# Kernel optimization log

Hardware: AMD Instinct MI355X
Metric: run time of the kernel (lower is better)

The kernel has to match this reference:

```python
import jax, jax.numpy as jnp
import numpy as np

D = 256; NH = 8; NL = 4; NP = 4; DFF = 1024
SHAPES = [(100, 100), (50, 50), (25, 25), (13, 13)]
B = 4


def layer_norm(x, g, b, eps=1e-5):
    m = x.mean(-1, keepdims=True)
    v = ((x - m) ** 2).mean(-1, keepdims=True)
    return (x - m) * jax.lax.rsqrt(v + eps) * g + b


def setup_inputs() -> dict:
    key = jax.random.key(0)
    ks = jax.random.split(key, 12)
    Lin = sum(h * w for h, w in SHAPES)  # 13294
    w = lambda k, s: jax.random.normal(k, s, jnp.float32) * 0.02
    return dict(
        src=jax.random.normal(ks[0], (B, Lin, D), jnp.float32),
        pos=0.1 * jax.random.normal(ks[1], (B, Lin, D), jnp.float32),
        reference_points=jax.random.uniform(ks[2], (B, Lin, NL, 2), dtype=jnp.float32),
        spatial_shapes=jnp.array(SHAPES, jnp.int32),
        level_start_index=jnp.array(np.cumsum([0] + [h * w for h, w in SHAPES])[:-1], jnp.int32),
        value_w=w(ks[3], (D, D)), value_b=jnp.zeros((D,), jnp.float32),
        offs_w=w(ks[4], (D, NH * NL * NP * 2)),
        offs_b=0.5 * jax.random.normal(ks[5], (NH * NL * NP * 2,), jnp.float32),
        attn_w=w(ks[6], (D, NH * NL * NP)), attn_b=jnp.zeros((NH * NL * NP,), jnp.float32),
        out_w=w(ks[7], (D, D)), out_b=jnp.zeros((D,), jnp.float32),
        ln1_g=jnp.ones((D,), jnp.float32), ln1_b=jnp.zeros((D,), jnp.float32),
        ff1_w=w(ks[8], (D, DFF)), ff1_b=jnp.zeros((DFF,), jnp.float32),
        ff2_w=w(ks[9], (DFF, D)), ff2_b=jnp.zeros((D,), jnp.float32),
        ln2_g=jnp.ones((D,), jnp.float32), ln2_b=jnp.zeros((D,), jnp.float32),
    )


def msda(query, value_in, ref, shapes, starts, value_w, value_b, offs_w, offs_b,
         attn_w, attn_b, out_w, out_b):
    Bq, Lq, Dm = query.shape
    dh = Dm // NH
    shapes_np = np.asarray(shapes); starts_np = np.asarray(starts)
    value = (value_in @ value_w + value_b).reshape(Bq, -1, NH, dh)
    offs = (query @ offs_w + offs_b).reshape(Bq, Lq, NH, NL, NP, 2)
    aw = jax.nn.softmax((query @ attn_w + attn_b).reshape(Bq, Lq, NH, NL * NP), axis=-1)
    aw = aw.reshape(Bq, Lq, NH, NL, NP)
    # offset normalizer is (W, H) per level
    normalizer = jnp.stack([shapes[:, 1], shapes[:, 0]], -1).astype(jnp.float32)
    loc = ref[:, :, None, :, None, :] + offs / normalizer[None, None, None, :, None, :]
    out = jnp.zeros((Bq, NH, Lq, dh), jnp.float32)
    for l in range(NL):
        Hl, Wl = int(shapes_np[l, 0]), int(shapes_np[l, 1])
        s = int(starts_np[l])
        v = value[:, s:s + Hl * Wl].transpose(0, 2, 1, 3)  # [B,h,HW,dh]
        x = loc[:, :, :, l, :, 0] * Wl - 0.5  # [B,Lq,h,P], align_corners=False
        y = loc[:, :, :, l, :, 1] * Hl - 0.5
        x0 = jnp.floor(x); y0 = jnp.floor(y)
        dx = x - x0; dy = y - y0
        x0i = x0.astype(jnp.int32); y0i = y0.astype(jnp.int32)
        def gather(ix, iy):
            valid = (ix >= 0) & (ix < Wl) & (iy >= 0) & (iy < Hl)  # zero padding
            idx = jnp.clip(iy, 0, Hl - 1) * Wl + jnp.clip(ix, 0, Wl - 1)
            idx = idx.transpose(0, 2, 1, 3).reshape(Bq, NH, Lq * NP)
            g = jnp.take_along_axis(v, idx[..., None], axis=2).reshape(Bq, NH, Lq, NP, dh)
            return g * valid.transpose(0, 2, 1, 3)[..., None]
        dxh = dx.transpose(0, 2, 1, 3)[..., None]
        dyh = dy.transpose(0, 2, 1, 3)[..., None]
        sampled = (gather(x0i, y0i) * (1 - dxh) * (1 - dyh)
                   + gather(x0i + 1, y0i) * dxh * (1 - dyh)
                   + gather(x0i, y0i + 1) * (1 - dxh) * dyh
                   + gather(x0i + 1, y0i + 1) * dxh * dyh)  # [B,h,Lq,P,dh]
        awl = aw[:, :, :, l].transpose(0, 2, 1, 3)[..., None]  # [B,h,Lq,P,1]
        out = out + (sampled * awl).sum(3)
    out = out.transpose(0, 2, 1, 3).reshape(Bq, Lq, Dm)
    return out @ out_w + out_b


def reference(src, pos, reference_points, spatial_shapes, level_start_index,
              value_w, value_b, offs_w, offs_b, attn_w, attn_b, out_w, out_b,
              ln1_g, ln1_b, ff1_w, ff1_b, ff2_w, ff2_b, ln2_g, ln2_b):
    # src = with_pos_embed(src, pos): NOTE this module uses (src + pos) as BOTH query and value
    q = src + pos
    src2 = msda(q, q, reference_points, spatial_shapes, level_start_index,
                value_w, value_b, offs_w, offs_b, attn_w, attn_b, out_w, out_b)
    x = layer_norm(q + src2, ln1_g, ln1_b)  # dropout is identity at eval
    ff = jnp.maximum(x @ ff1_w + ff1_b, 0.0) @ ff2_w + ff2_b
    return layer_norm(x + ff, ln2_g, ln2_b)
```

## Files before the change

kernel.cpp:

```cpp
#include <hip/hip_runtime.h>
#include <hip/hip_bf16.h>

#define B_    4
#define LIN   13294
#define M_    (B_*LIN)
#define D_    256
#define NH_   8
#define NL_   4
#define NP_   4
#define DFF_  1024

typedef __bf16 bf16;
typedef unsigned int uint;
typedef __attribute__((ext_vector_type(8))) __bf16 bfrag8;
typedef __attribute__((ext_vector_type(4))) __bf16 bf16x4;
typedef __attribute__((ext_vector_type(4))) float facc4;
typedef __attribute__((ext_vector_type(2))) float f32x2;

__global__ __launch_bounds__(256) void make_q(const float* __restrict__ src,
                                              const float* __restrict__ pos,
                                              float* __restrict__ q,
                                              bf16* __restrict__ qb, int n4) {
  int i = blockIdx.x * 256 + threadIdx.x;
  if (i >= n4) return;
  float4 s = ((const float4*)src)[i];
  float4 p = ((const float4*)pos)[i];
  float4 v = {s.x + p.x, s.y + p.y, s.z + p.z, s.w + p.w};
  ((float4*)q)[i] = v;
  bf16 t4[4] = {(bf16)v.x, (bf16)v.y, (bf16)v.z, (bf16)v.w};
  ((uint2*)qb)[i] = *(uint2*)t4;
}

__global__ __launch_bounds__(256) void prep_weights(
    const float* __restrict__ vw, const float* __restrict__ ow,
    const float* __restrict__ aw, const float* __restrict__ outw,
    const float* __restrict__ f1w, const float* __restrict__ f2w,
    const float* __restrict__ ob, const float* __restrict__ ab,
    bf16* __restrict__ vwt, bf16* __restrict__ oawt, bf16* __restrict__ outwt,
    bf16* __restrict__ f1wt, bf16* __restrict__ f2wt, float* __restrict__ oabias) {
  int seg = blockIdx.y;
  int idx = blockIdx.x * 256 + threadIdx.x;
  if (seg == 6) {
    if (idx < 256) oabias[idx] = ob[idx];
    else if (idx < 384) oabias[idx] = ab[idx - 256];
    return;
  }
  const float* W; bf16* Wt; int K, N;
  switch (seg) {
    case 0: W = vw;   Wt = vwt;          K = 256;  N = 256;  break;
    case 1: W = ow;   Wt = oawt;         K = 256;  N = 256;  break;
    case 2: W = aw;   Wt = oawt + 65536; K = 256;  N = 128;  break;
    case 3: W = outw; Wt = outwt;        K = 256;  N = 256;  break;
    case 4: W = f1w;  Wt = f1wt;         K = 256;  N = 1024; break;
    default: W = f2w; Wt = f2wt;         K = 1024; N = 256;  break;
  }
  if (idx < K * N) {
    int n = idx / K, k = idx - n * K;
    Wt[idx] = (bf16)W[k * N + n];
  }
}

__device__ __forceinline__ void gload16(const void* g, void* l) {
  __builtin_amdgcn_global_load_lds(
      (const __attribute__((address_space(1))) uint*)g,
      (__attribute__((address_space(3))) uint*)l, 16, 0, 0);
}

template<bool RELU>
__global__ __launch_bounds__(256) void gemm128(
    const bf16* __restrict__ A, const bf16* __restrict__ Bt,
    const float* __restrict__ bias, bf16* __restrict__ C,
    int Mdim, int K, int N) {
  __shared__ __align__(16) bf16 As[128 * 64];
  __shared__ __align__(16) bf16 Bs[128 * 64];
  const int t = threadIdx.x, wave = t >> 6, lane = t & 63;
  const int m0 = blockIdx.x * 128, n0 = blockIdx.y * 128;
  const int wr = wave >> 1, wc = wave & 1;
  const int ln = lane & 15, quad = lane >> 4;
  const int sr = lane >> 3, cc = lane & 7;
  const int gcol = (cc ^ sr) * 8;

  const bf16* aptr[4]; const bf16* bptr[4];
  bf16* alds[4]; bf16* blds[4];
  #pragma unroll
  for (int ii = 0; ii < 4; ii++) {
    int i = wave * 4 + ii;
    int arow = min(m0 + i * 8 + sr, Mdim - 1);
    aptr[ii] = A + (size_t)arow * K + gcol;
    bptr[ii] = Bt + (size_t)(n0 + i * 8 + sr) * K + gcol;
    alds[ii] = As + i * 512;
    blds[ii] = Bs + i * 512;
  }
  int a_off[2][4], b_off[2][4];
  #pragma unroll
  for (int ks = 0; ks < 2; ks++) {
    int gc = ks * 4 + quad;
    #pragma unroll
    for (int rt = 0; rt < 4; rt++) {
      int ra = wr * 64 + rt * 16 + ln;
      int rb = wc * 64 + rt * 16 + ln;
      a_off[ks][rt] = ra * 128 + ((gc ^ (ra & 7)) * 16);
      b_off[ks][rt] = rb * 128 + ((gc ^ (rb & 7)) * 16);
    }
  }

  facc4 acc[4][4];
  facc4 z = {0.f, 0.f, 0.f, 0.f};
  #pragma unroll
  for (int rt = 0; rt < 4; rt++)
    #pragma unroll
    for (int ct = 0; ct < 4; ct++) acc[rt][ct] = z;

  for (int k0 = 0; k0 < K; k0 += 64) {
    __syncthreads();
    #pragma unroll
    for (int ii = 0; ii < 4; ii++) gload16(aptr[ii] + k0, alds[ii]);
    #pragma unroll
    for (int ii = 0; ii < 4; ii++) gload16(bptr[ii] + k0, blds[ii]);
    __syncthreads();
    #pragma unroll
    for (int ks = 0; ks < 2; ks++) {
      bfrag8 afr[4], bfr[4];
      #pragma unroll
      for (int ct = 0; ct < 4; ct++)
        bfr[ct] = *(const bfrag8*)((const char*)Bs + b_off[ks][ct]);
      #pragma unroll
      for (int rt = 0; rt < 4; rt++)
        afr[rt] = *(const bfrag8*)((const char*)As + a_off[ks][rt]);
      #pragma unroll
      for (int rt = 0; rt < 4; rt++)
        #pragma unroll
        for (int ct = 0; ct < 4; ct++)
          acc[rt][ct] = __builtin_amdgcn_mfma_f32_16x16x32_bf16(afr[rt], bfr[ct], acc[rt][ct], 0, 0, 0);
    }
  }

  #pragma unroll
  for (int ct = 0; ct < 4; ct++) {
    int col = n0 + wc * 64 + ct * 16 + ln;
    float bv = bias[col];
    #pragma unroll
    for (int rt = 0; rt < 4; rt++) {
      #pragma unroll
      for (int reg = 0; reg < 4; reg++) {
        int row = m0 + wr * 64 + rt * 16 + quad * 4 + reg;
        if (row < Mdim) {
          float v = acc[rt][ct][reg] + bv;
          if (RELU) v = fmaxf(v, 0.f);
          C[(size_t)row * N + col] = (bf16)v;
        }
      }
    }
  }
}

__global__ __launch_bounds__(256) void msda_sample(
    const bf16* __restrict__ value,
    const bf16* __restrict__ OA,
    const float* __restrict__ ref,
    bf16* __restrict__ sampled) {
  int gw = (blockIdx.x * 256 + threadIdx.x) >> 6;
  int lane = threadIdx.x & 63;
  int m = gw >> 3, h = gw & 7;
  if (m >= M_) return;
  int b = m / LIN;
  int p = lane >> 2, cg = lane & 3;
  int l = p >> 2, pt = p & 3;
  int Wl = (l == 0) ? 100 : (l == 1) ? 50 : (l == 2) ? 25 : 13;
  int Hl = Wl;
  int st = (l == 0) ? 0 : (l == 1) ? 10000 : (l == 2) ? 12500 : 13125;

  float logit = (float)OA[(size_t)m * 384 + 256 + h * 16 + p];
  float mx = logit;
  #pragma unroll
  for (int msk = 4; msk < 64; msk <<= 1) mx = fmaxf(mx, __shfl_xor(mx, msk));
  float e = __expf(logit - mx);
  float se = e;
  #pragma unroll
  for (int msk = 4; msk < 64; msk <<= 1) se += __shfl_xor(se, msk);
  float w = e / se;

  float rx = ref[((size_t)m * 4 + l) * 2 + 0];
  float ry = ref[((size_t)m * 4 + l) * 2 + 1];
  float ox = (float)OA[(size_t)m * 384 + ((h * 4 + l) * 4 + pt) * 2 + 0];
  float oy = (float)OA[(size_t)m * 384 + ((h * 4 + l) * 4 + pt) * 2 + 1];
  float x = rx * (float)Wl + ox - 0.5f;
  float y = ry * (float)Hl + oy - 0.5f;
  float x0f = floorf(x), y0f = floorf(y);
  float dx = x - x0f, dy = y - y0f;
  int x0 = (int)x0f, y0 = (int)y0f;
  float wx1 = 1.f - dx, wy1 = 1.f - dy;

  f32x2 acc2[4];
  #pragma unroll
  for (int t = 0; t < 4; t++) acc2[t] = (f32x2){0.f, 0.f};

  size_t vbase = ((size_t)(b * LIN + st)) * 256 + h * 32 + cg * 8;
  #pragma unroll
  for (int c = 0; c < 4; c++) {
    int cx = c & 1, cy = c >> 1;
    int xi = x0 + cx, yi = y0 + cy;
    bool valid = (xi >= 0) & (xi < Wl) & (yi >= 0) & (yi < Hl);
    int xc = min(max(xi, 0), Wl - 1);
    int yc = min(max(yi, 0), Hl - 1);
    float cw = (cx ? dx : wx1) * (cy ? dy : wy1) * w;
    cw = valid ? cw : 0.f;
    uint off = (uint)(yc * Wl + xc) * 256u;
    const uint4 vv = *(const uint4*)(value + vbase + off);
    f32x2 cw2 = {cw, cw};
    f32x2 v0 = {__uint_as_float(vv.x << 16), __uint_as_float(vv.x & 0xffff0000u)};
    f32x2 v1 = {__uint_as_float(vv.y << 16), __uint_as_float(vv.y & 0xffff0000u)};
    f32x2 v2 = {__uint_as_float(vv.z << 16), __uint_as_float(vv.z & 0xffff0000u)};
    f32x2 v3 = {__uint_as_float(vv.w << 16), __uint_as_float(vv.w & 0xffff0000u)};
    acc2[0] = cw2 * v0 + acc2[0];
    acc2[1] = cw2 * v1 + acc2[1];
    acc2[2] = cw2 * v2 + acc2[2];
    acc2[3] = cw2 * v3 + acc2[3];
  }

  int sel = (lane >> 2) & 1;
  f32x2 sA0 = sel ? acc2[0] : acc2[2];
  f32x2 sA1 = sel ? acc2[1] : acc2[3];
  f32x2 kA0 = sel ? acc2[2] : acc2[0];
  f32x2 kA1 = sel ? acc2[3] : acc2[1];
  f32x2 rA0, rA1;
  rA0.x = __shfl_xor(sA0.x, 4); rA0.y = __shfl_xor(sA0.y, 4);
  rA1.x = __shfl_xor(sA1.x, 4); rA1.y = __shfl_xor(sA1.y, 4);
  kA0 += rA0; kA1 += rA1;

  int sel2 = (lane >> 3) & 1;
  f32x2 sB = sel2 ? kA0 : kA1;
  f32x2 kB = sel2 ? kA1 : kA0;
  f32x2 rB;
  rB.x = __shfl_xor(sB.x, 8); rB.y = __shfl_xor(sB.y, 8);
  kB += rB;

  int sel3 = (lane >> 4) & 1;
  float sC = sel3 ? kB.x : kB.y;
  float kC = sel3 ? kB.y : kB.x;
  kC += __shfl_xor(sC, 16);

  float v = kC + __shfl_xor(kC, 32);

  if (lane < 32) {
    int c = cg * 8 + ((lane >> 2) & 1) * 4 + ((lane >> 3) & 1) * 2 + ((lane >> 4) & 1);
    sampled[(size_t)m * 256 + h * 32 + c] = (bf16)v;
  }
}

__device__ inline float4 load4f(const float* p) { return *(const float4*)p; }
__device__ inline float4 load4f(const bf16* p) {
  bf16x4 v = *(const bf16x4*)p;
  float4 r = {(float)v[0], (float)v[1], (float)v[2], (float)v[3]};
  return r;
}
template<typename RT>
__global__ __launch_bounds__(256) void ln_kernel(
    const bf16* __restrict__ a, const RT* __restrict__ res,
    const float* __restrict__ g, const float* __restrict__ beta,
    float* __restrict__ out_f, bf16* __restrict__ out_b, int Mdim) {
  int wave = threadIdx.x >> 6, lane = threadIdx.x & 63;
  int row = blockIdx.x * 4 + wave;
  if (row >= Mdim) return;
  size_t base = (size_t)row * 256 + lane * 4;
  float4 av = load4f(a + base);
  float4 rv = load4f(res + base);
  float4 v = {av.x + rv.x, av.y + rv.y, av.z + rv.z, av.w + rv.w};
  float s = v.x + v.y + v.z + v.w;
  #pragma unroll
  for (int msk = 1; msk < 64; msk <<= 1) s += __shfl_xor(s, msk);
  float mean = s * (1.f / 256.f);
  float4 d = {v.x - mean, v.y - mean, v.z - mean, v.w - mean};
  float sq = d.x * d.x + d.y * d.y + d.z * d.z + d.w * d.w;
  #pragma unroll
  for (int msk = 1; msk < 64; msk <<= 1) sq += __shfl_xor(sq, msk);
  float inv = rsqrtf(sq * (1.f / 256.f) + 1e-5f);
  float4 gv = *(const float4*)(g + lane * 4);
  float4 bv = *(const float4*)(beta + lane * 4);
  float4 y = {d.x * inv * gv.x + bv.x, d.y * inv * gv.y + bv.y,
              d.z * inv * gv.z + bv.z, d.w * inv * gv.w + bv.w};
  if (out_f) *(float4*)(out_f + base) = y;
  if (out_b) {
    bf16 t4[4] = {(bf16)y.x, (bf16)y.y, (bf16)y.z, (bf16)y.w};
    *(uint2*)(out_b + base) = *(uint2*)t4;
  }
}

extern "C" void kernel_launch(void* const* d_in, const int* in_sizes, int n_in,
                              void* d_out, int out_size, void* d_ws, size_t ws_size,
                              hipStream_t stream) {
  const float* src     = (const float*)d_in[0];
  const float* pos     = (const float*)d_in[1];
  const float* refpts  = (const float*)d_in[2];
  const float* value_w = (const float*)d_in[5];
  const float* value_b = (const float*)d_in[6];
  const float* offs_w  = (const float*)d_in[7];
  const float* offs_b  = (const float*)d_in[8];
  const float* attn_w  = (const float*)d_in[9];
  const float* attn_b  = (const float*)d_in[10];
  const float* out_w   = (const float*)d_in[11];
  const float* out_b   = (const float*)d_in[12];
  const float* ln1_g   = (const float*)d_in[13];
  const float* ln1_b   = (const float*)d_in[14];
  const float* ff1_w   = (const float*)d_in[15];
  const float* ff1_b   = (const float*)d_in[16];
  const float* ff2_w   = (const float*)d_in[17];
  const float* ff2_b   = (const float*)d_in[18];
  const float* ln2_g   = (const float*)d_in[19];
  const float* ln2_b   = (const float*)d_in[20];

  char* ws = (char*)d_ws;
  size_t off = 0;
  auto take = [&](size_t bytes) -> char* {
    char* pp = ws + off;
    off += (bytes + 255) & ~(size_t)255;
    return pp;
  };
  float* q      = (float*)take((size_t)M_ * 256 * 4);
  size_t szQB   = (size_t)M_ * 256 * 2;
  size_t szOA   = (size_t)M_ * 384 * 2;
  char* R       = take(szQB * 3 + szOA);
  bf16* qb      = (bf16*)R;
  bf16* valueb  = (bf16*)(R + szQB);
  bf16* OA      = (bf16*)(R + 2 * szQB);
  bf16* sampled = (bf16*)(R + 2 * szQB + szOA);
  bf16* hb      = (bf16*)R;
  bf16* tmp     = (bf16*)take(szQB);
  bf16* x       = (bf16*)take(szQB);
  bf16* vwt     = (bf16*)take(65536 * 2);
  bf16* oawt    = (bf16*)take(98304 * 2);
  bf16* outwt   = (bf16*)take(65536 * 2);
  bf16* f1wt    = (bf16*)take(262144 * 2);
  bf16* f2wt    = (bf16*)take(262144 * 2);
  float* oabias = (float*)take(384 * 4);
  (void)ws_size; (void)in_sizes; (void)n_in; (void)out_size;

  int n4 = M_ * 256 / 4;
  make_q<<<dim3((n4 + 255) / 256), dim3(256), 0, stream>>>(src, pos, q, qb, n4);
  prep_weights<<<dim3(1024, 7), dim3(256), 0, stream>>>(
      value_w, offs_w, attn_w, out_w, ff1_w, ff2_w, offs_b, attn_b,
      vwt, oawt, outwt, f1wt, f2wt, oabias);

  dim3 blk(256);
  int mt = (M_ + 127) / 128;
  gemm128<false><<<dim3(mt, 2), blk, 0, stream>>>(qb, vwt, value_b, valueb, M_, 256, 256);
  gemm128<false><<<dim3(mt, 3), blk, 0, stream>>>(qb, oawt, oabias, OA, M_, 256, 384);
  msda_sample<<<dim3(M_ * 2), blk, 0, stream>>>(valueb, OA, refpts, sampled);
  gemm128<false><<<dim3(mt, 2), blk, 0, stream>>>(sampled, outwt, out_b, tmp, M_, 256, 256);
  ln_kernel<float><<<dim3((M_ + 3) / 4), blk, 0, stream>>>(tmp, q, ln1_g, ln1_b, nullptr, x, M_);
  gemm128<true><<<dim3(mt, 8), blk, 0, stream>>>(x, f1wt, ff1_b, hb, M_, 256, 1024);
  gemm128<false><<<dim3(mt, 2), blk, 0, stream>>>(hb, f2wt, ff2_b, tmp, M_, 1024, 256);
  ln_kernel<bf16><<<dim3((M_ + 3) / 4), blk, 0, stream>>>(tmp, x, ln2_g, ln2_b, (float*)d_out, nullptr, M_);
}
```

Before: 672.7 us.

## Fuse value and offset/attention projections into one GEMM, vectorize GEMM stores

Concatenates the value, sampling-offset and attention-logit weights into a single 640-column projection, so the query activations are read once by one GEMM launch instead of two. The sampling kernel then reads value, offsets and logits from the shared 640-wide rows, and loads each x/y offset pair as one 32-bit word. The GEMM now takes K as a template constant and swaps the MFMA operand order so each lane holds four consecutive output columns, which allows 8-byte bf16 stores and float4 bias loads. Softmax drops the max-subtraction, which saves two shuffle reductions but could overflow if logits are large. The wider row stride spreads value rows further apart in memory, which may hurt cache locality in the gather.

```diff
diff --git a/kernel.cpp b/kernel.cpp
--- a/kernel.cpp
+++ b/kernel.cpp
@@ -35,24 +35,26 @@
     const float* __restrict__ vw, const float* __restrict__ ow,
     const float* __restrict__ aw, const float* __restrict__ outw,
     const float* __restrict__ f1w, const float* __restrict__ f2w,
-    const float* __restrict__ ob, const float* __restrict__ ab,
-    bf16* __restrict__ vwt, bf16* __restrict__ oawt, bf16* __restrict__ outwt,
-    bf16* __restrict__ f1wt, bf16* __restrict__ f2wt, float* __restrict__ oabias) {
+    const float* __restrict__ vb, const float* __restrict__ ob,
+    const float* __restrict__ ab,
+    bf16* __restrict__ vowt, bf16* __restrict__ outwt,
+    bf16* __restrict__ f1wt, bf16* __restrict__ f2wt, float* __restrict__ vobias) {
   int seg = blockIdx.y;
   int idx = blockIdx.x * 256 + threadIdx.x;
   if (seg == 6) {
-    if (idx < 256) oabias[idx] = ob[idx];
-    else if (idx < 384) oabias[idx] = ab[idx - 256];
+    if (idx < 256) vobias[idx] = vb[idx];
+    else if (idx < 512) vobias[idx] = ob[idx - 256];
+    else if (idx < 640) vobias[idx] = ab[idx - 512];
     return;
   }
   const float* W; bf16* Wt; int K, N;
   switch (seg) {
-    case 0: W = vw;   Wt = vwt;          K = 256;  N = 256;  break;
-    case 1: W = ow;   Wt = oawt;         K = 256;  N = 256;  break;
-    case 2: W = aw;   Wt = oawt + 65536; K = 256;  N = 128;  break;
-    case 3: W = outw; Wt = outwt;        K = 256;  N = 256;  break;
-    case 4: W = f1w;  Wt = f1wt;         K = 256;  N = 1024; break;
-    default: W = f2w; Wt = f2wt;         K = 1024; N = 256;  break;
+    case 0: W = vw;   Wt = vowt;              K = 256;  N = 256;  break;
+    case 1: W = ow;   Wt = vowt + 256 * 256;  K = 256;  N = 256;  break;
+    case 2: W = aw;   Wt = vowt + 512 * 256;  K = 256;  N = 128;  break;
+    case 3: W = outw; Wt = outwt;             K = 256;  N = 256;  break;
+    case 4: W = f1w;  Wt = f1wt;              K = 256;  N = 1024; break;
+    default: W = f2w; Wt = f2wt;              K = 1024; N = 256;  break;
   }
   if (idx < K * N) {
     int n = idx / K, k = idx - n * K;
@@ -60,17 +62,17 @@
   }
 }
 
-__device__ __forceinline__ void gload16(const void* g, void* l) {
+__device__ __forceinline__ void gload16(const bf16* g, bf16* l) {
   __builtin_amdgcn_global_load_lds(
       (const __attribute__((address_space(1))) uint*)g,
       (__attribute__((address_space(3))) uint*)l, 16, 0, 0);
 }
 
-template<bool RELU>
+template<int K, bool RELU>
 __global__ __launch_bounds__(256) void gemm128(
     const bf16* __restrict__ A, const bf16* __restrict__ Bt,
     const float* __restrict__ bias, bf16* __restrict__ C,
-    int Mdim, int K, int N) {
+    int Mdim, int N) {
   __shared__ __align__(16) bf16 As[128 * 64];
   __shared__ __align__(16) bf16 Bs[128 * 64];
   const int t = threadIdx.x, wave = t >> 6, lane = t & 63;
@@ -80,83 +82,80 @@
   const int sr = lane >> 3, cc = lane & 7;
   const int gcol = (cc ^ sr) * 8;
 
-  const bf16* aptr[4]; const bf16* bptr[4];
-  bf16* alds[4]; bf16* blds[4];
+  const bf16* ap[4]; const bf16* bp[4];
+  bf16* la[4]; bf16* lb[4];
   #pragma unroll
   for (int ii = 0; ii < 4; ii++) {
     int i = wave * 4 + ii;
     int arow = min(m0 + i * 8 + sr, Mdim - 1);
-    aptr[ii] = A + (size_t)arow * K + gcol;
-    bptr[ii] = Bt + (size_t)(n0 + i * 8 + sr) * K + gcol;
-    alds[ii] = As + i * 512;
-    blds[ii] = Bs + i * 512;
-  }
-  int a_off[2][4], b_off[2][4];
-  #pragma unroll
-  for (int ks = 0; ks < 2; ks++) {
-    int gc = ks * 4 + quad;
+    ap[ii] = A + (size_t)arow * K + gcol;
+    bp[ii] = Bt + (size_t)(n0 + i * 8 + sr) * K + gcol;
+    la[ii] = As + i * 512;
+    lb[ii] = Bs + i * 512;
+  }
+  int a_off[4], b_off[4];
+  #pragma unroll
+  for (int i = 0; i < 4; i++) {
+    int ra = wr * 64 + i * 16 + ln;
+    int rb = wc * 64 + i * 16 + ln;
+    a_off[i] = ra * 128 + ((quad ^ (ra & 7)) * 16);
+    b_off[i] = rb * 128 + ((quad ^ (rb & 7)) * 16);
+  }
+
+  facc4 acc[4][4];
+  #pragma unroll
+  for (int mt = 0; mt < 4; mt++)
     #pragma unroll
-    for (int rt = 0; rt < 4; rt++) {
-      int ra = wr * 64 + rt * 16 + ln;
-      int rb = wc * 64 + rt * 16 + ln;
-      a_off[ks][rt] = ra * 128 + ((gc ^ (ra & 7)) * 16);
-      b_off[ks][rt] = rb * 128 + ((gc ^ (rb & 7)) * 16);
-    }
-  }
-
-  facc4 acc[4][4];
-  facc4 z = {0.f, 0.f, 0.f, 0.f};
-  #pragma unroll
-  for (int rt = 0; rt < 4; rt++)
-    #pragma unroll
-    for (int ct = 0; ct < 4; ct++) acc[rt][ct] = z;
-
+    for (int nt = 0; nt < 4; nt++) acc[mt][nt] = (facc4){0.f, 0.f, 0.f, 0.f};
+
+  #pragma unroll 1
   for (int k0 = 0; k0 < K; k0 += 64) {
     __syncthreads();
-    #pragma unroll
-    for (int ii = 0; ii < 4; ii++) gload16(aptr[ii] + k0, alds[ii]);
-    #pragma unroll
-    for (int ii = 0; ii < 4; ii++) gload16(bptr[ii] + k0, blds[ii]);
+    gload16(ap[0] + k0, la[0]); gload16(ap[1] + k0, la[1]);
+    gload16(ap[2] + k0, la[2]); gload16(ap[3] + k0, la[3]);
+    gload16(bp[0] + k0, lb[0]); gload16(bp[1] + k0, lb[1]);
+    gload16(bp[2] + k0, lb[2]); gload16(bp[3] + k0, lb[3]);
     __syncthreads();
     #pragma unroll
     for (int ks = 0; ks < 2; ks++) {
-      bfrag8 afr[4], bfr[4];
+      bfrag8 wfr[4], xfr[4];
       #pragma unroll
-      for (int ct = 0; ct < 4; ct++)
-        bfr[ct] = *(const bfrag8*)((const char*)Bs + b_off[ks][ct]);
+      for (int nt = 0; nt < 4; nt++)
+        wfr[nt] = *(const bfrag8*)((const char*)Bs + (b_off[nt] ^ (ks * 64)));
       #pragma unroll
-      for (int rt = 0; rt < 4; rt++)
-        afr[rt] = *(const bfrag8*)((const char*)As + a_off[ks][rt]);
+      for (int mt = 0; mt < 4; mt++)
+        xfr[mt] = *(const bfrag8*)((const char*)As + (a_off[mt] ^ (ks * 64)));
       #pragma unroll
-      for (int rt = 0; rt < 4; rt++)
+      for (int mt = 0; mt < 4; mt++)
         #pragma unroll
-        for (int ct = 0; ct < 4; ct++)
-          acc[rt][ct] = __builtin_amdgcn_mfma_f32_16x16x32_bf16(afr[rt], bfr[ct], acc[rt][ct], 0, 0, 0);
+        for (int nt = 0; nt < 4; nt++)
+          acc[mt][nt] = __builtin_amdgcn_mfma_f32_16x16x32_bf16(wfr[nt], xfr[mt], acc[mt][nt], 0, 0, 0);
     }
   }
 
   #pragma unroll
-  for (int ct = 0; ct < 4; ct++) {
-    int col = n0 + wc * 64 + ct * 16 + ln;
-    float bv = bias[col];
+  for (int nt = 0; nt < 4; nt++) {
+    int ncol = n0 + wc * 64 + nt * 16 + quad * 4;
+    float4 bv = *(const float4*)&bias[ncol];
     #pragma unroll
-    for (int rt = 0; rt < 4; rt++) {
-      #pragma unroll
-      for (int reg = 0; reg < 4; reg++) {
-        int row = m0 + wr * 64 + rt * 16 + quad * 4 + reg;
-        if (row < Mdim) {
-          float v = acc[rt][ct][reg] + bv;
-          if (RELU) v = fmaxf(v, 0.f);
-          C[(size_t)row * N + col] = (bf16)v;
+    for (int mt = 0; mt < 4; mt++) {
+      int row = m0 + wr * 64 + mt * 16 + ln;
+      if (row < Mdim) {
+        float v0 = acc[mt][nt][0] + bv.x, v1 = acc[mt][nt][1] + bv.y;
+        float v2 = acc[mt][nt][2] + bv.z, v3 = acc[mt][nt][3] + bv.w;
+        if (RELU) {
+          v0 = fmaxf(v0, 0.f); v1 = fmaxf(v1, 0.f);
+          v2 = fmaxf(v2, 0.f); v3 = fmaxf(v3, 0.f);
         }
+        bf16 o[4] = {(bf16)v0, (bf16)v1, (bf16)v2, (bf16)v3};
+        *(uint2*)&C[(size_t)row * N + ncol] = *(uint2*)o;
       }
     }
   }
 }
 
 __global__ __launch_bounds__(256) void msda_sample(
-    const bf16* __restrict__ value,
-    const bf16* __restrict__ OA,
+    const bf16* __restrict__ VOA,
     const float* __restrict__ ref,
     bf16* __restrict__ sampled) {
   int gw = (blockIdx.x * 256 + threadIdx.x) >> 6;
@@ -170,11 +169,8 @@
   int Hl = Wl;
   int st = (l == 0) ? 0 : (l == 1) ? 10000 : (l == 2) ? 12500 : 13125;
 
-  float logit = (float)OA[(size_t)m * 384 + 256 + h * 16 + p];
-  float mx = logit;
-  #pragma unroll
-  for (int msk = 4; msk < 64; msk <<= 1) mx = fmaxf(mx, __shfl_xor(mx, msk));
-  float e = __expf(logit - mx);
+  const bf16* row = VOA + (size_t)m * 640;
+  float e = __expf((float)row[512 + h * 16 + p]);
   float se = e;
   #pragma unroll
   for (int msk = 4; msk < 64; msk <<= 1) se += __shfl_xor(se, msk);
@@ -182,8 +178,9 @@
 
   float rx = ref[((size_t)m * 4 + l) * 2 + 0];
   float ry = ref[((size_t)m * 4 + l) * 2 + 1];
-  float ox = (float)OA[(size_t)m * 384 + ((h * 4 + l) * 4 + pt) * 2 + 0];
-  float oy = (float)OA[(size_t)m * 384 + ((h * 4 + l) * 4 + pt) * 2 + 1];
+  uint oxy = *(const uint*)&row[256 + ((h * 4 + l) * 4 + pt) * 2];
+  float ox = __uint_as_float(oxy << 16);
+  float oy = __uint_as_float(oxy & 0xffff0000u);
   float x = rx * (float)Wl + ox - 0.5f;
   float y = ry * (float)Hl + oy - 0.5f;
   float x0f = floorf(x), y0f = floorf(y);
@@ -193,9 +190,9 @@
 
   f32x2 acc2[4];
   #pragma unroll
-  for (int t = 0; t < 4; t++) acc2[t] = (f32x2){0.f, 0.f};
-
-  size_t vbase = ((size_t)(b * LIN + st)) * 256 + h * 32 + cg * 8;
+  for (int i = 0; i < 4; i++) acc2[i] = (f32x2){0.f, 0.f};
+
+  size_t vbase = ((size_t)(b * LIN + st)) * 640 + h * 32 + cg * 8;
   #pragma unroll
   for (int c = 0; c < 4; c++) {
     int cx = c & 1, cy = c >> 1;
@@ -205,8 +202,8 @@
     int yc = min(max(yi, 0), Hl - 1);
     float cw = (cx ? dx : wx1) * (cy ? dy : wy1) * w;
     cw = valid ? cw : 0.f;
-    uint off = (uint)(yc * Wl + xc) * 256u;
-    const uint4 vv = *(const uint4*)(value + vbase + off);
+    uint off = (uint)(yc * Wl + xc) * 640u;
+    const uint4 vv = *(const uint4*)(VOA + vbase + off);
     f32x2 cw2 = {cw, cw};
     f32x2 v0 = {__uint_as_float(vv.x << 16), __uint_as_float(vv.x & 0xffff0000u)};
     f32x2 v1 = {__uint_as_float(vv.y << 16), __uint_as_float(vv.y & 0xffff0000u)};
@@ -318,37 +315,34 @@
   };
   float* q      = (float*)take((size_t)M_ * 256 * 4);
   size_t szQB   = (size_t)M_ * 256 * 2;
-  size_t szOA   = (size_t)M_ * 384 * 2;
-  char* R       = take(szQB * 3 + szOA);
+  size_t szVOA  = (size_t)M_ * 640 * 2;
+  char* R       = take(szQB + szVOA + szQB);
   bf16* qb      = (bf16*)R;
-  bf16* valueb  = (bf16*)(R + szQB);
-  bf16* OA      = (bf16*)(R + 2 * szQB);
-  bf16* sampled = (bf16*)(R + 2 * szQB + szOA);
+  bf16* VOA     = (bf16*)(R + szQB);
+  bf16* sampled = (bf16*)(R + szQB + szVOA);
   bf16* hb      = (bf16*)R;
   bf16* tmp     = (bf16*)take(szQB);
   bf16* x       = (bf16*)take(szQB);
-  bf16* vwt     = (bf16*)take(65536 * 2);
-  bf16* oawt    = (bf16*)take(98304 * 2);
+  bf16* vowt    = (bf16*)take(640 * 256 * 2);
   bf16* outwt   = (bf16*)take(65536 * 2);
   bf16* f1wt    = (bf16*)take(262144 * 2);
   bf16* f2wt    = (bf16*)take(262144 * 2);
-  float* oabias = (float*)take(384 * 4);
+  float* vobias = (float*)take(640 * 4);
   (void)ws_size; (void)in_sizes; (void)n_in; (void)out_size;
 
   int n4 = M_ * 256 / 4;
   make_q<<<dim3((n4 + 255) / 256), dim3(256), 0, stream>>>(src, pos, q, qb, n4);
   prep_weights<<<dim3(1024, 7), dim3(256), 0, stream>>>(
-      value_w, offs_w, attn_w, out_w, ff1_w, ff2_w, offs_b, attn_b,
-      vwt, oawt, outwt, f1wt, f2wt, oabias);
+      value_w, offs_w, attn_w, out_w, ff1_w, ff2_w, value_b, offs_b, attn_b,
+      vowt, outwt, f1wt, f2wt, vobias);
 
   dim3 blk(256);
   int mt = (M_ + 127) / 128;
-  gemm128<false><<<dim3(mt, 2), blk, 0, stream>>>(qb, vwt, value_b, valueb, M_, 256, 256);
-  gemm128<false><<<dim3(mt, 3), blk, 0, stream>>>(qb, oawt, oabias, OA, M_, 256, 384);
-  msda_sample<<<dim3(M_ * 2), blk, 0, stream>>>(valueb, OA, refpts, sampled);
-  gemm128<false><<<dim3(mt, 2), blk, 0, stream>>>(sampled, outwt, out_b, tmp, M_, 256, 256);
+  gemm128<256, false><<<dim3(mt, 5), blk, 0, stream>>>(qb, vowt, vobias, VOA, M_, 640);
+  msda_sample<<<dim3(M_ * 2), blk, 0, stream>>>(VOA, refpts, sampled);
+  gemm128<256, false><<<dim3(mt, 2), blk, 0, stream>>>(sampled, outwt, out_b, tmp, M_, 256);
   ln_kernel<float><<<dim3((M_ + 3) / 4), blk, 0, stream>>>(tmp, q, ln1_g, ln1_b, nullptr, x, M_);
-  gemm128<true><<<dim3(mt, 8), blk, 0, stream>>>(x, f1wt, ff1_b, hb, M_, 256, 1024);
-  gemm128<false><<<dim3(mt, 2), blk, 0, stream>>>(hb, f2wt, ff2_b, tmp, M_, 1024, 256);
+  gemm128<256, true><<<dim3(mt, 8), blk, 0, stream>>>(x, f1wt, ff1_b, hb, M_, 1024);
+  gemm128<1024, false><<<dim3(mt, 2), blk, 0, stream>>>(hb, f2wt, ff2_b, tmp, M_, 256);
   ln_kernel<bf16><<<dim3((M_ + 3) / 4), blk, 0, stream>>>(tmp, x, ln2_g, ln2_b, (float*)d_out, nullptr, M_);
 }
```

New measurement: 582.3 us. -13.4%, faster.
